# Kernel optimization log

Hardware: AMD Instinct MI355X
Metric: run time of the kernel (lower is better)

The kernel has to match this reference:

```python
import jax, jax.numpy as jnp
import numpy as np

N_H = 896
N_EMB = 300
V_IN = 30000
V_OUT = 30000
B = 64
T_ENC = 40
T_DEC = 40


def gru_cell(x, h, Wih, Whh, bih, bhh):
    # PyTorch GRU cell math
    gi = x @ Wih.T + bih          # [B, 3H]
    gh = h @ Whh.T + bhh          # [B, 3H]
    ir, iz, inn = jnp.split(gi, 3, axis=-1)
    hr, hz, hn = jnp.split(gh, 3, axis=-1)
    r = jax.nn.sigmoid(ir + hr)
    z = jax.nn.sigmoid(iz + hz)
    n = jnp.tanh(inn + r * hn)
    return (1.0 - z) * n + z * h


def run_gru(xs, h0, Wih, Whh, bih, bhh, reverse=False):
    # xs: [T, B, E] -> outputs [T, B, H], final hidden [B, H]
    def step(h, x):
        h2 = gru_cell(x, h, Wih, Whh, bih, bhh)
        return h2, h2
    hT, ys = jax.lax.scan(step, h0, xs, reverse=reverse)
    return ys, hT


def setup_inputs() -> dict:
    key = jax.random.key(0)
    ks = jax.random.split(key, 20)
    s = 0.05
    inp = {
        'x_encoder': jax.random.randint(ks[0], (B, T_ENC), 0, V_IN - 1),
        'x_decoder': jax.random.randint(ks[1], (B, T_DEC), 0, V_OUT - 1),
        'emb_enc': jax.random.normal(ks[2], (V_IN, N_EMB), jnp.float32) * s,
        'Wih_f': jax.random.normal(ks[3], (3 * N_H, N_EMB), jnp.float32) * s,
        'Whh_f': jax.random.normal(ks[4], (3 * N_H, N_H), jnp.float32) * s,
        'bih_f': jnp.zeros((3 * N_H,), jnp.float32),
        'bhh_f': jnp.zeros((3 * N_H,), jnp.float32),
        'Wih_b': jax.random.normal(ks[5], (3 * N_H, N_EMB), jnp.float32) * s,
        'Whh_b': jax.random.normal(ks[6], (3 * N_H, N_H), jnp.float32) * s,
        'bih_b': jnp.zeros((3 * N_H,), jnp.float32),
        'bhh_b': jnp.zeros((3 * N_H,), jnp.float32),
        'emb_dec': jax.random.normal(ks[7], (V_OUT, N_EMB), jnp.float32) * s,
        'Wih_d': jax.random.normal(ks[8], (3 * N_H, N_EMB), jnp.float32) * s,
        'Whh_d': jax.random.normal(ks[9], (3 * N_H, N_H), jnp.float32) * s,
        'bih_d': jnp.zeros((3 * N_H,), jnp.float32),
        'bhh_d': jnp.zeros((3 * N_H,), jnp.float32),
        'fc_W': jax.random.normal(ks[10], (V_OUT, 2 * N_H), jnp.float32) * s,
        'fc_b': jnp.zeros((V_OUT,), jnp.float32),
    }
    return inp


def reference(x_encoder, x_decoder, emb_enc, Wih_f, Whh_f, bih_f, bhh_f,
              Wih_b, Whh_b, bih_b, bhh_b, emb_dec, Wih_d, Whh_d, bih_d,
              bhh_d, fc_W, fc_b):
    Bsz = x_encoder.shape[0]
    h0 = jnp.zeros((Bsz, N_H), jnp.float32)

    # ---- Encoder: bidirectional 1-layer GRU (no padding, full lengths) ----
    xs = emb_enc[x_encoder].transpose(1, 0, 2)          # [Te, B, E]
    y_f, h_f = run_gru(xs, h0, Wih_f, Whh_f, bih_f, bhh_f)
    y_b, h_b = run_gru(xs, h0, Wih_b, Whh_b, bih_b, bhh_b, reverse=True)
    y_enc = (y_f + y_b).transpose(1, 0, 2)              # [B, Te, H] (dirs summed)
    h = h_f + h_b                                       # [B, H]

    # ---- Decoder: per-step GRU + dot-product attention over encoder ----
    xd = emb_dec[x_decoder].transpose(1, 0, 2)          # [Td, B, E]

    def dec_step(h, x):
        h2 = gru_cell(x, h, Wih_d, Whh_d, bih_d, bhh_d)        # [B, H]
        scores = jnp.einsum('bth,bh->bt', y_enc, h2)           # ed_mat
        attn = jax.nn.softmax(scores, axis=1)                  # over Te
        ctx = jnp.einsum('bt,bth->bh', attn, y_enc)            # [B, H]
        logits = jnp.concatenate([h2, ctx], axis=-1) @ fc_W.T + fc_b
        return h2, jax.nn.softmax(logits, axis=-1)

    _, ys = jax.lax.scan(dec_step, h, xd)               # [Td, B, V]
    return ys.transpose(1, 0, 2)                        # [B, Td, V]
```

## Files before the change

### kernel.cpp

```cpp
#include <hip/hip_runtime.h>

#define BB 64
#define TE 40
#define TD 40
#define ED 300
#define EP 320
#define HD 896
#define G3 2688
#define VO 30000
#define VP2 30208
#define KZ 1792
#define KT 28
#define MR 2560
#define NBLK 120
#define NWB 248
#define NTN 118
#define NTILE (NTN * 10)

#define FOFF 0
#define BOFF 56
#define DOFF 112
#define AOFF 168
#define TOFF 232
#define ZOFF 352
#define QOFF 448
#define FWC  456
#define MTO  464
#define QSO  496
#define FSTR 32

typedef __attribute__((ext_vector_type(8))) __bf16 bf16x8;
typedef __attribute__((ext_vector_type(4))) float f32x4;
typedef __attribute__((ext_vector_type(4))) unsigned int u32x4;
typedef __attribute__((ext_vector_type(4))) unsigned short u16x4;

typedef __attribute__((address_space(1))) const void av1c;
typedef __attribute__((address_space(3))) void av3;

__device__ __forceinline__ float sig_(float x)  { return 1.0f / (1.0f + __expf(-x)); }
__device__ __forceinline__ float tanh_(float x) { return 1.0f - 2.0f / (__expf(2.0f * x) + 1.0f); }

__device__ __forceinline__ void gload_lds16(const __bf16* g, __bf16* l) {
    __builtin_amdgcn_global_load_lds((av1c*)g, (av3*)l, 16, 0, 0);
}
__device__ __forceinline__ void gload_lds16_sc(const __bf16* g, __bf16* l) {
    __builtin_amdgcn_global_load_lds((av1c*)g, (av3*)l, 16, 0, 17);
}

__device__ __forceinline__ bf16x8 ld128_sc(const __bf16* p) {
    bf16x8 r;
    asm volatile("global_load_dwordx4 %0, %1, off sc0 sc1" : "=v"(r) : "v"(p));
    return r;
}
__device__ __forceinline__ f32x4 ldf4_sc(const float* p) {
    f32x4 r;
    asm volatile("global_load_dwordx4 %0, %1, off sc0 sc1" : "=v"(r) : "v"(p));
    return r;
}
__device__ __forceinline__ float ldf_sc(const float* p) {
    float r;
    asm volatile("global_load_dword %0, %1, off sc0 sc1" : "=v"(r) : "v"(p));
    return r;
}
__device__ __forceinline__ void vm_wait0() {
    asm volatile("s_waitcnt vmcnt(0)" ::: "memory");
}
__device__ __forceinline__ void stf_sc(float* p, float v) {
    asm volatile("global_store_dword %0, %1, off sc0 sc1" :: "v"(p), "v"(v) : "memory");
}
__device__ __forceinline__ void sth_sc(__bf16* p, float v) {
    unsigned int u = (unsigned int)__builtin_bit_cast(unsigned short, (__bf16)v);
    asm volatile("global_store_short %0, %1, off sc0 sc1" :: "v"(p), "v"(u) : "memory");
}
__device__ __forceinline__ void st8_sc(__bf16* p, u16x4 v) {
    asm volatile("global_store_dwordx2 %0, %1, off sc0 sc1" :: "v"(p), "v"(v) : "memory");
}
__device__ __forceinline__ void sti_sc(int* p, int v) {
    asm volatile("global_store_dword %0, %1, off sc0 sc1" :: "v"(p), "v"(v) : "memory");
}
__device__ __forceinline__ void spin_ge(const int* p, int target) {
    int v;
    for (;;) {
        asm volatile("global_load_dword %0, %1, off sc0 sc1\n\ts_waitcnt vmcnt(0)"
                     : "=v"(v) : "v"(p) : "memory");
        if (v >= target) break;
        __builtin_amdgcn_s_sleep(1);
    }
}
__device__ __forceinline__ void spinb(const int* p, int target) {
    for (int it = 0; it < (1 << 20); ++it) {
        int v;
        asm volatile("global_load_dword %0, %1, off sc0 sc1\n\ts_waitcnt vmcnt(0)"
                     : "=v"(v) : "v"(p) : "memory");
        if (v >= target) return;
        __builtin_amdgcn_s_sleep(16);
    }
}

__device__ __forceinline__ size_t hblk(int b, int c) {
    return ((size_t)(c >> 4) * 64 + b) * 16 + (c & 15);
}

__device__ __forceinline__ void stage_w(__bf16* wlds, const float* __restrict__ W, int c0)
{
    const int tid = threadIdx.x;
    for (int ch = tid; ch < 48 * 224; ch += 256) {
        const int lr = ch / 224, c4 = (ch % 224) * 4;
        const int g = lr >> 4, rr = lr & 15;
        const int kk = c4 >> 5, hi = (c4 & 31) >> 3, j = c4 & 7;
        const float4 v = *(const float4*)&W[(size_t)(g * HD + c0 + rr) * HD + c4];
        __bf16* d = &wlds[((g * 28 + kk) * 64 + hi * 16 + rr) * 8 + j];
        d[0] = (__bf16)v.x; d[1] = (__bf16)v.y; d[2] = (__bf16)v.z; d[3] = (__bf16)v.w;
    }
}

struct GiReg { float g0[4], g1[4], g2[4]; };

__device__ __forceinline__ GiReg gi_prefetch(const float* __restrict__ GIt,
                                             int c, int w, int hi)
{
    GiReg r;
#pragma unroll
    for (int rg = 0; rg < 4; ++rg) {
        const float* gp = GIt + (size_t)(16 * w + hi * 4 + rg) * G3 + c;
        r.g0[rg] = gp[0]; r.g1[rg] = gp[HD]; r.g2[rg] = gp[2 * HD];
    }
    return r;
}

__device__ __forceinline__ void gru_step(
    const __bf16* __restrict__ hcurB, const float* __restrict__ hcurF,
    const __bf16* __restrict__ wlds, const GiReg& gi,
    float bh0, float bh1, float bh2,
    float* __restrict__ hnF, __bf16* __restrict__ hnB,
    float* __restrict__ yencD, int tt,
    __bf16* __restrict__ zrow,
    int c0, int lane, int w)
{
    const int r16 = lane & 15, hi = lane >> 4;
    const int c = c0 + r16;
    const int colblk = c0 >> 4;
    const int brow = 16 * w;

    bf16x8 afr[28];
    const __bf16* ap = hcurB + ((size_t)(hi >> 1) * 64 + brow + r16) * 16 + (hi & 1) * 8;
#pragma unroll
    for (int kk = 0; kk < 28; ++kk) afr[kk] = ld128_sc(ap + kk * 2048);
    float hp[4];
#pragma unroll
    for (int rg = 0; rg < 4; ++rg)
        hp[rg] = ldf_sc(hcurF + ((size_t)colblk * 64 + brow + hi * 4 + rg) * 16 + r16);
    vm_wait0();
    __builtin_amdgcn_sched_barrier(0);

    f32x4 a0 = {0.f, 0.f, 0.f, 0.f}, a1 = a0, a2 = a0;
#pragma unroll
    for (int kk = 0; kk < 28; ++kk) {
        const bf16x8 b0 = *(const bf16x8*)&wlds[(kk) * 512 + lane * 8];
        const bf16x8 b1 = *(const bf16x8*)&wlds[(28 + kk) * 512 + lane * 8];
        const bf16x8 b2 = *(const bf16x8*)&wlds[(56 + kk) * 512 + lane * 8];
        a0 = __builtin_amdgcn_mfma_f32_16x16x32_bf16(afr[kk], b0, a0, 0, 0, 0);
        a1 = __builtin_amdgcn_mfma_f32_16x16x32_bf16(afr[kk], b1, a1, 0, 0, 0);
        a2 = __builtin_amdgcn_mfma_f32_16x16x32_bf16(afr[kk], b2, a2, 0, 0, 0);
    }

#pragma unroll
    for (int rg = 0; rg < 4; ++rg) {
        const int b = brow + hi * 4 + rg;
        const float rr = sig_(gi.g0[rg] + a0[rg] + bh0);
        const float zz = sig_(gi.g1[rg] + a1[rg] + bh1);
        const float nn = tanh_(gi.g2[rg] + rr * (a2[rg] + bh2));
        const float hnew = (1.0f - zz) * nn + zz * hp[rg];
        const size_t so = ((size_t)colblk * 64 + b) * 16 + r16;
        stf_sc(hnF + so, hnew);
        sth_sc(hnB + so, hnew);
        if (yencD) stf_sc(yencD + (((size_t)colblk * 64 + b) * TE + tt) * 16 + r16, hnew);
        if (zrow)  sth_sc(zrow + (size_t)b * KZ + c, hnew);
    }
}

__device__ __forceinline__ void attn_step512(
    const float* __restrict__ yencL, float* __restrict__ h2s,
    float* __restrict__ scL, float* __restrict__ attwL,
    const float* __restrict__ h2g, int b, __bf16* __restrict__ zr,
    int* __restrict__ myflag, int* __restrict__ zflag, int postval)
{
    const int tid = threadIdx.x, lane = tid & 63, w = tid >> 6;

    float a0 = 0.f, a1 = 0.f;
    if (tid < HD) a0 = ldf_sc(h2g + hblk(b, tid));
    if (tid + 512 < HD) a1 = ldf_sc(h2g + hblk(b, tid + 512));
    vm_wait0();
    __builtin_amdgcn_sched_barrier(0);
    if (tid < HD) h2s[tid] = a0;
    if (tid + 512 < HD) h2s[tid + 512] = a1;
    __syncthreads();
    if (tid == 0) sti_sc(myflag, postval);

    const float2* h22 = (const float2*)h2s;
    for (int t = w; t < TE; t += 8) {
        const float2* y2 = (const float2*)(yencL + t * HD);
        float p = 0.f;
#pragma unroll
        for (int it = 0; it < HD / 128; ++it) {
            const float2 ya = y2[lane + it * 64];
            const float2 hb2 = h22[lane + it * 64];
            p += ya.x * hb2.x + ya.y * hb2.y;
        }
        p += __shfl_down(p, 32); p += __shfl_down(p, 16); p += __shfl_down(p, 8);
        p += __shfl_down(p, 4);  p += __shfl_down(p, 2);  p += __shfl_down(p, 1);
        if (lane == 0) scL[t] = p;
    }
    __syncthreads();

    float m = scL[0];
    for (int t = 1; t < TE; ++t) m = fmaxf(m, scL[t]);
    float s = 0.f;
    for (int t = 0; t < TE; ++t) s += __expf(scL[t] - m);
    const float inv = 1.0f / s;
    if (tid < TE) attwL[tid] = __expf(scL[tid] - m) * inv;
    __syncthreads();

    for (int c = tid; c < HD; c += 512) {
        float acc = 0.f;
#pragma unroll
        for (int t = 0; t < TE; ++t) acc += attwL[t] * yencL[t * HD + c];
        sth_sc(zr + (size_t)b * KZ + HD + c, acc);
    }
    vm_wait0();
    __syncthreads();
    if (tid == 0) sti_sc(zflag, postval);
}

__device__ __forceinline__ void softmax512(float* row, float* red, float* red2,
                                           float* __restrict__ orow)
{
    const int tid = threadIdx.x, lane = tid & 63, w = tid >> 6;

    for (int it = 0; it < 3; ++it) {
        f32x4 v[5]; int jj[5]; bool ok[5];
#pragma unroll
        for (int u = 0; u < 5; ++u) {
            jj[u] = it * 2560 + u * 512 + tid;
            ok[u] = jj[u] < VO / 4;
            if (ok[u]) v[u] = ldf4_sc(orow + (size_t)jj[u] * 4);
        }
        vm_wait0();
        __builtin_amdgcn_sched_barrier(0);
#pragma unroll
        for (int u = 0; u < 5; ++u)
            if (ok[u]) *(f32x4*)&row[(size_t)jj[u] * 4] = v[u];
    }
    __syncthreads();

    float m = -1e30f;
    for (int ch = tid; ch < VO / 4; ch += 512) {
        const f32x4 x = *(const f32x4*)&row[ch * 4];
        m = fmaxf(fmaxf(fmaxf(m, x[0]), x[1]), fmaxf(x[2], x[3]));
    }
    m = fmaxf(m, __shfl_down(m, 32)); m = fmaxf(m, __shfl_down(m, 16));
    m = fmaxf(m, __shfl_down(m, 8));  m = fmaxf(m, __shfl_down(m, 4));
    m = fmaxf(m, __shfl_down(m, 2));  m = fmaxf(m, __shfl_down(m, 1));
    if (lane == 0) red[w] = m;
    __syncthreads();
    if (tid == 0) {
        float mm = red[0];
#pragma unroll
        for (int i = 1; i < 8; ++i) mm = fmaxf(mm, red[i]);
        red[0] = mm;
    }
    __syncthreads();
    m = red[0];

    float s = 0.0f;
    for (int v2 = tid; v2 < VO; v2 += 512) {
        const float e = __expf(row[v2] - m);
        row[v2] = e;
        s += e;
    }
    s += __shfl_down(s, 32); s += __shfl_down(s, 16); s += __shfl_down(s, 8);
    s += __shfl_down(s, 4);  s += __shfl_down(s, 2);  s += __shfl_down(s, 1);
    if (lane == 0) red2[w] = s;
    __syncthreads();
    if (tid == 0) {
        float ss = red2[0];
#pragma unroll
        for (int i = 1; i < 8; ++i) ss += red2[i];
        red2[0] = ss;
    }
    __syncthreads();
    s = red2[0];

    const float inv = 1.0f / s;
    for (int ch = tid; ch < VO / 4; ch += 512) {
        f32x4 x = *(const f32x4*)&row[ch * 4];
        x[0] *= inv; x[1] *= inv; x[2] *= inv; x[3] *= inv;
        *(f32x4*)&orow[(size_t)ch * 4] = x;
    }
    __syncthreads();
}

__global__ __launch_bounds__(512, 1) void recur(
    const float* __restrict__ GIf, const float* __restrict__ GIb,
    const float* __restrict__ GId,
    const float* __restrict__ WhhF, const float* __restrict__ WhhB,
    const float* __restrict__ WhhD,
    const float* __restrict__ bhhF, const float* __restrict__ bhhB,
    const float* __restrict__ bhhD,
    float* __restrict__ heF, __bf16* __restrict__ heB,
    float* __restrict__ hdF, __bf16* __restrict__ hdB,
    float* __restrict__ yenc_f, float* __restrict__ yenc_b,
    __bf16* __restrict__ Zb, int* __restrict__ flags,
    const float* __restrict__ fcWsrc, __bf16* __restrict__ fcW,
    float* __restrict__ outC, const float* __restrict__ fcb)
{
    __shared__ __align__(16) char smem[147456];
    __bf16* wlds  = (__bf16*)smem;
    float*  yencL = (float*)smem;
    float*  h2s   = (float*)(smem + 143360);
    float*  scL   = (float*)(smem + 146944);
    float*  attwL = (float*)(smem + 147136);
    float*  redA  = (float*)(smem + 131072);
    float*  redB  = (float*)(smem + 131136);
    volatile int* shtile = (volatile int*)(smem + 147400);

    const int gid = blockIdx.x;
    const int tid = threadIdx.x;
    const int lane = tid & 63, w = tid >> 6;
    const int r16 = lane & 15, hi = lane >> 4;
    const size_t S = (size_t)BB * HD;

    if (gid < NBLK) {
        float bb0 = 0.f, bb1 = 0.f, bb2 = 0.f;
        GiReg gi;

        if (gid < 112) {
            const int dir = (gid >= 56) ? 1 : 0;
            const int gloc = dir ? gid - 56 : gid;
            const int c0e = gloc * 16;
            const float* GIe  = dir ? GIb : GIf;
            const float* bhhE = dir ? bhhB : bhhF;
            float* yencD = dir ? yenc_b : yenc_f;
            const int foff = dir ? BOFF : FOFF;
            const int ce = c0e + r16;

            stage_w(wlds, dir ? WhhB : WhhF, c0e);
            if (tid < 256) {
                bb0 = bhhE[ce]; bb1 = bhhE[HD + ce]; bb2 = bhhE[2 * HD + ce];
                gi = gi_prefetch(GIe + (size_t)(dir ? TE - 1 : 0) * BB * G3, ce, w, hi);
            }
            __syncthreads();

            for (int t = 0; t < TE; ++t) {
                if (t > 0) {
                    if (tid < 56) spin_ge(flags + (foff + tid) * FSTR, t);
                    __syncthreads();
                }
                const int tt = dir ? (TE - 1 - t) : t;
                if (tid < 256)
                    gru_step(heB + (size_t)(dir * 2 + (t & 1)) * S,
                             heF + (size_t)(dir * 2 + (t & 1)) * S,
                             wlds, gi, bb0, bb1, bb2,
                             heF + (size_t)(dir * 2 + ((t + 1) & 1)) * S,
                             heB + (size_t)(dir * 2 + ((t + 1) & 1)) * S,
                             yencD, tt, nullptr, c0e, lane, w);
                vm_wait0();
                __syncthreads();
                if (tid == 0) sti_sc(flags + (foff + gloc) * FSTR, t + 1);
                if (t + 1 < TE && tid < 256) {
                    const int ttn = dir ? (TE - 2 - t) : (t + 1);
                    gi = gi_prefetch(GIe + (size_t)ttn * BB * G3, ce, w, hi);
                }
            }
        }

        if (tid < 112) spin_ge(flags + tid * FSTR, TE);
        __syncthreads();

        {
            const int i0 = gid * 256 + tid;
            const int i1 = i0 + NBLK * 256;
            const bool has0 = (i0 < BB * HD);
            const bool has1 = (i1 < BB * HD);
            const float f0 = has0 ? ldf_sc(&heF[0 * S + i0]) : 0.f;
            const float b0 = has0 ? ldf_sc(&heF[2 * S + i0]) : 0.f;
            const float f1 = has1 ? ldf_sc(&heF[0 * S + i1]) : 0.f;
            const float b1 = has1 ? ldf_sc(&heF[2 * S + i1]) : 0.f;
            vm_wait0();
            __builtin_amdgcn_sched_barrier(0);
            if (has0) { const float v0 = f0 + b0; stf_sc(&hdF[i0], v0); sth_sc(&hdB[i0], v0); }
            if (has1) { const float v1 = f1 + b1; stf_sc(&hdF[i1], v1); sth_sc(&hdB[i1], v1); }
        }
        if (gid < 56) {
            stage_w(wlds, WhhD, gid * 16);
            if (tid < 256) {
                const int cd = gid * 16 + r16;
                bb0 = bhhD[cd]; bb1 = bhhD[HD + cd]; bb2 = bhhD[2 * HD + cd];
                gi = gi_prefetch(GId, cd, w, hi);
            }
        }
        vm_wait0();
        __syncthreads();
        if (tid == 0) sti_sc(flags + (TOFF + gid) * FSTR, 1);
        if (tid < 120) spin_ge(flags + (TOFF + tid) * FSTR, 1);
        __syncthreads();

        if (gid < 56) {
            for (int p = 0; p < TD; ++p) {
                if (p > 0 && tid < 56) spin_ge(flags + (DOFF + tid) * FSTR, p);
                if (p >= 4 && tid >= 64 && tid < 128)
                    spin_ge(flags + (AOFF + tid - 64) * FSTR, p - 3);
                __syncthreads();
                if (tid < 256)
                    gru_step(hdB + (size_t)(p & 3) * S, hdF + (size_t)(p & 3) * S,
                             wlds, gi, bb0, bb1, bb2,
                             hdF + (size_t)((p + 1) & 3) * S, hdB + (size_t)((p + 1) & 3) * S,
                             nullptr, 0, Zb + (size_t)p * BB * KZ, gid * 16, lane, w);
                vm_wait0();
                __syncthreads();
                if (tid == 0) sti_sc(flags + (DOFF + gid) * FSTR, p + 1);
                if (p + 1 < TD && tid < 256)
                    gi = gi_prefetch(GId + (size_t)(p + 1) * BB * G3, gid * 16 + r16, w, hi);
            }
        } else {
            const int b = gid - 56;
            const float* sf = yenc_f;
            const float* sb = yenc_b;
            for (int it = 0; it < 4; ++it) {
                f32x4 a_[5], b_[5];
                int tt_[5], gg_[5], cc_[5]; bool ok[5];
#pragma unroll
                for (int u = 0; u < 5; ++u) {
                    const int j = it * 2560 + u * 512 + tid;
                    ok[u] = (j < 8960);
                    if (ok[u]) {
                        gg_[u] = j / 160;
                        const int rem = j - gg_[u] * 160;
                        tt_[u] = rem >> 2;
                        cc_[u] = (rem & 3) * 4;
                        const size_t sa = (((size_t)gg_[u] * 64 + b) * TE + tt_[u]) * 16 + cc_[u];
                        a_[u] = ldf4_sc(sf + sa);
                        b_[u] = ldf4_sc(sb + sa);
                    }
                }
                vm_wait0();
                __builtin_amdgcn_sched_barrier(0);
#pragma unroll
                for (int u = 0; u < 5; ++u)
                    if (ok[u])
                        *(f32x4*)&yencL[(size_t)tt_[u] * HD + gg_[u] * 16 + cc_[u]] = a_[u] + b_[u];
            }
            __syncthreads();
            for (int s = 0; s < TD; ++s) {
                if (tid < 56) spin_ge(flags + (DOFF + tid) * FSTR, s + 1);
                __syncthreads();
                attn_step512(yencL, h2s, scL, attwL, hdF + (size_t)((s + 1) & 3) * S,
                             b, Zb + (size_t)s * BB * KZ,
                             flags + (AOFF + b) * FSTR, flags + (ZOFF + b) * FSTR, s + 1);
            }
        }
    } else {
        const int slice = gid - NBLK;
        const size_t base = (size_t)slice * 236 * KZ;
        const int nf4 = 236 * KZ / 4;
        for (int i = tid; i < nf4; i += 512) {
            const size_t e0 = base + (size_t)i * 4;
            const int r = (int)(e0 / KZ);
            u16x4 o;
            if (r < VO) {
                const float4 x = *(const float4*)&fcWsrc[e0];
                o.x = __builtin_bit_cast(unsigned short, (__bf16)x.x);
                o.y = __builtin_bit_cast(unsigned short, (__bf16)x.y);
                o.z = __builtin_bit_cast(unsigned short, (__bf16)x.z);
                o.w = __builtin_bit_cast(unsigned short, (__bf16)x.w);
            } else {
                o.x = 0; o.y = 0; o.z = 0; o.w = 0;
            }
            st8_sc(&fcW[e0], o);
        }
        vm_wait0();
        __syncthreads();
        if (tid == 0)
            __hip_atomic_fetch_add(flags + FWC * FSTR, 1, __ATOMIC_RELAXED,
                                   __HIP_MEMORY_SCOPE_AGENT);
    }

    {
        __bf16* lds = (__bf16*)smem;
        const int wave = tid >> 6;
        const int wm = wave >> 2, wn = wave & 3;
        int* qcnt = flags + QOFF * FSTR;

        if (tid == 0) spinb(flags + FWC * FSTR, 128);
        __syncthreads();

        const int srow0 = wave * 8 + (lane >> 3);
        const int scol  = ((lane & 7) ^ (lane >> 3)) * 8;
        const int cbx0 = ((hi * 16) ^ ((r16 & 7) << 4)) >> 1;
        const int cbx1 = ((64 + hi * 16) ^ ((r16 & 7) << 4)) >> 1;

        for (;;) {
            if (tid == 0) {
                const int tl = __hip_atomic_fetch_add(qcnt, 1, __ATOMIC_RELAXED,
                                                      __HIP_MEMORY_SCOPE_AGENT);
                *shtile = tl;
            }
            __syncthreads();
            const int tile = *shtile;
            if (tile >= NTILE) break;
            const int mt = tile / NTN, nt = tile - mt * NTN;
            const int need = 4 * mt + 4;
            if (tid < 56) spinb(flags + (DOFF + tid) * FSTR, need);
            if (tid >= 64 && tid < 128) spinb(flags + (ZOFF + tid - 64) * FSTR, need);
            __syncthreads();

            const long tileM = (long)mt * 256;
            const long tileN = (long)nt * 256;
            const __bf16* gAh[2] = { Zb + (size_t)tileM * KZ, Zb + (size_t)(tileM + 128) * KZ };
            const __bf16* gBh[2] = { fcW + (size_t)tileN * KZ, fcW + (size_t)(tileN + 128) * KZ };
            auto Abase = [](int buf, int h) { return (buf * 2 + h) * 8192; };
            auto Bbase = [](int buf, int h) { return 32768 + (buf * 2 + h) * 8192; };
            auto stageA = [&](const __bf16* gph, int kt, int lbase) {
                const __bf16* g0 = gph + (size_t)srow0 * KZ + kt * 64 + scol;
                gload_lds16_sc(g0, &lds[lbase + wave * 512]);
                gload_lds16_sc(g0 + (size_t)64 * KZ, &lds[lbase + (8 + wave) * 512]);
            };
            auto stageB = [&](const __bf16* gph, int kt, int lbase) {
                const __bf16* g0 = gph + (size_t)srow0 * KZ + kt * 64 + scol;
                gload_lds16(g0, &lds[lbase + wave * 512]);
                gload_lds16(g0 + (size_t)64 * KZ, &lds[lbase + (8 + wave) * 512]);
            };

            f32x4 acc[8][4];
            const f32x4 zero = {0.f, 0.f, 0.f, 0.f};
#pragma unroll
            for (int m = 0; m < 8; ++m)
#pragma unroll
                for (int n = 0; n < 4; ++n) acc[m][n] = zero;

            stageA(gAh[0], 0, Abase(0, 0));
            stageA(gAh[1], 0, Abase(0, 1));
            stageB(gBh[0], 0, Bbase(0, 0));
            stageB(gBh[1], 0, Bbase(0, 1));
            stageB(gBh[0], 1, Bbase(1, 0));
            stageB(gBh[1], 1, Bbase(1, 1));
            asm volatile("s_waitcnt vmcnt(4)" ::: "memory");
            __builtin_amdgcn_s_barrier();

            for (int kt = 0; kt < KT; ++kt) {
                const int buf = kt & 1;
                const int kn1 = (kt + 1 < KT) ? kt + 1 : 0;
                const int kn2 = (kt + 2 < KT) ? kt + 2 : 0;
                const int Ab = Abase(buf, wm);
                const int Bb = Bbase(buf, wn >> 1);
                bf16x8 bfr[4][2];
#pragma unroll
                for (int q = 0; q < 4; ++q) {
                    if (q == 0) {
#pragma unroll
                        for (int n = 0; n < 4; ++n) {
                            const int rowB = (wn & 1) * 64 + n * 16 + r16;
                            bfr[n][0] = *(const bf16x8*)&lds[Bb + rowB * 64 + cbx0];
                            bfr[n][1] = *(const bf16x8*)&lds[Bb + rowB * 64 + cbx1];
                        }
                    }
                    bf16x8 af[2][2];
#pragma unroll
                    for (int mm = 0; mm < 2; ++mm) {
                        const int rowA = (q * 2 + mm) * 16 + r16;
                        af[mm][0] = *(const bf16x8*)&lds[Ab + rowA * 64 + cbx0];
                        af[mm][1] = *(const bf16x8*)&lds[Ab + rowA * 64 + cbx1];
                    }
                    if (q == 0)      stageA(gAh[0], kn1, Abase(buf ^ 1, 0));
                    else if (q == 1) stageA(gAh[1], kn1, Abase(buf ^ 1, 1));
                    else if (q == 2) stageB(gBh[0], kn2, Bbase(buf, 0));
                    else {
                        stageB(gBh[1], kn2, Bbase(buf, 1));
                        asm volatile("s_waitcnt vmcnt(4)" ::: "memory");
                    }
                    __builtin_amdgcn_s_barrier();
                    asm volatile("s_waitcnt lgkmcnt(0)" ::: "memory");
                    __builtin_amdgcn_sched_barrier(0);
                    __builtin_amdgcn_s_setprio(1);
#pragma unroll
                    for (int mm = 0; mm < 2; ++mm)
#pragma unroll
                        for (int n = 0; n < 4; ++n) {
                            acc[q * 2 + mm][n] = __builtin_amdgcn_mfma_f32_16x16x32_bf16(
                                af[mm][0], bfr[n][0], acc[q * 2 + mm][n], 0, 0, 0);
                            acc[q * 2 + mm][n] = __builtin_amdgcn_mfma_f32_16x16x32_bf16(
                                af[mm][1], bfr[n][1], acc[q * 2 + mm][n], 0, 0, 0);
                        }
                    __builtin_amdgcn_s_setprio(0);
                    __builtin_amdgcn_sched_barrier(0);
                    __builtin_amdgcn_s_barrier();
                }
            }
            asm volatile("s_waitcnt vmcnt(0)" ::: "memory");

#pragma unroll
            for (int m = 0; m < 8; ++m) {
#pragma unroll
                for (int n = 0; n < 4; ++n) {
                    const long gcol = tileN + wn * 64 + n * 16 + r16;
                    if (gcol >= VO) continue;
                    const float bv = fcb[gcol];
#pragma unroll
                    for (int rr = 0; rr < 4; ++rr) {
                        const long grow = tileM + wm * 128 + m * 16 + hi * 4 + rr;
                        const long t = grow >> 6, b = grow & 63;
                        stf_sc(&outC[(b * TD + t) * VO + gcol], acc[m][n][rr] + bv);
                    }
                }
            }
            vm_wait0();
            __syncthreads();
            if (tid == 0)
                __hip_atomic_fetch_add(flags + (MTO + mt) * FSTR, 1, __ATOMIC_RELAXED,
                                       __HIP_MEMORY_SCOPE_AGENT);
            __syncthreads();
        }
    }

    {
        int* qs = flags + QSO * FSTR;
        for (;;) {
            if (tid == 0) {
                const int qv = __hip_atomic_fetch_add(qs, 1, __ATOMIC_RELAXED,
                                                      __HIP_MEMORY_SCOPE_AGENT);
                *shtile = qv;
            }
            __syncthreads();
            const int q = *shtile;
            if (q >= MR) break;
            const int mt = q >> 8;
            if (tid == 0) spinb(flags + (MTO + mt) * FSTR, NTN);
            __syncthreads();
            const int sub = q & 255;
            const int t = 4 * mt + (sub >> 6), b = sub & 63;
            softmax512((float*)smem, redA, redB, outC + (size_t)(b * TD + t) * VO);
        }
    }
}

__global__ __launch_bounds__(256) void gemm_bt(
    const __bf16* __restrict__ A0, const __bf16* __restrict__ B0,
    float* __restrict__ C0, const float* __restrict__ bias0,
    const __bf16* __restrict__ A1, const __bf16* __restrict__ B1,
    float* __restrict__ C1, const float* __restrict__ bias1,
    int M, int N, int K)
{
    constexpr int BM = 128, BN = 128, BK = 32;
    constexpr int FM = 4, FN = 4;

    const __bf16* A = A0; const __bf16* Bp = B0;
    float* C = C0; const float* bias = bias0;
    if (blockIdx.z == 1) { A = A1; Bp = B1; C = C1; bias = bias1; }

    __shared__ __bf16 Ash[2][BM * BK];
    __shared__ __bf16 Bsh[2][BN * BK];

    const int tid  = threadIdx.x;
    const int lane = tid & 63;
    const int wave = tid >> 6;
    const int wr = wave >> 1, wc = wave & 1;

    const int nwg = gridDim.x * gridDim.y;
    const int orig = blockIdx.y * gridDim.x + blockIdx.x;
    const int q = nwg >> 3, r = nwg & 7;
    const int xcd = orig & 7, idx = orig >> 3;
    const int wg = (xcd < r ? xcd * (q + 1) : r * (q + 1) + (xcd - r) * q) + idx;
    const int mtiles = gridDim.y;
    const long tileM = (long)(wg % mtiles) * BM;
    const long tileN = (long)(wg / mtiles) * BN;

    const int r16 = lane & 15;
    const int hi  = lane >> 4;

    f32x4 acc[FM][FN];
    const f32x4 zero = {0.f, 0.f, 0.f, 0.f};
#pragma unroll
    for (int m = 0; m < FM; ++m)
#pragma unroll
        for (int n = 0; n < FN; ++n) acc[m][n] = zero;

    const int srow = wave * 32 + (lane >> 2);
    const int schunk = (lane & 3) * 8;
    const __bf16* gA = A + (size_t)(tileM + srow) * K + schunk;
    const __bf16* gB = Bp + (size_t)(tileN + srow) * K + schunk;
    const size_t kstep16 = (size_t)16 * K;
    const int lofs = (wave * 32) * BK;

#define STAGE_T(k0_, sel_)                                            \
    do {                                                              \
        gload_lds16(gA + (k0_), &Ash[sel_][lofs]);                    \
        gload_lds16(gA + (k0_) + kstep16, &Ash[sel_][lofs + 16 * BK]);\
        gload_lds16(gB + (k0_), &Bsh[sel_][lofs]);                    \
        gload_lds16(gB + (k0_) + kstep16, &Bsh[sel_][lofs + 16 * BK]);\
    } while (0)

    STAGE_T(0, 0);
    int cur = 0;
    for (int k0 = BK; k0 < K; k0 += BK) {
        STAGE_T(k0, cur ^ 1);
        asm volatile("s_waitcnt vmcnt(4)" ::: "memory");
        __builtin_amdgcn_s_barrier();
        __builtin_amdgcn_sched_barrier(0);

        bf16x8 af[FM], bfr[FN];
#pragma unroll
        for (int m = 0; m < FM; ++m)
            af[m] = *(const bf16x8*)&Ash[cur][(wr * 64 + m * 16 + r16) * BK + hi * 8];
#pragma unroll
        for (int n = 0; n < FN; ++n)
            bfr[n] = *(const bf16x8*)&Bsh[cur][(wc * 64 + n * 16 + r16) * BK + hi * 8];
#pragma unroll
        for (int m = 0; m < FM; ++m)
#pragma unroll
            for (int n = 0; n < FN; ++n)
                acc[m][n] = __builtin_amdgcn_mfma_f32_16x16x32_bf16(af[m], bfr[n], acc[m][n], 0, 0, 0);

        __builtin_amdgcn_sched_barrier(0);
        __builtin_amdgcn_s_barrier();
        __builtin_amdgcn_sched_barrier(0);
        cur ^= 1;
    }
    asm volatile("s_waitcnt vmcnt(0)" ::: "memory");
    __builtin_amdgcn_s_barrier();
    __builtin_amdgcn_sched_barrier(0);
    {
        bf16x8 af[FM], bfr[FN];
#pragma unroll
        for (int m = 0; m < FM; ++m)
            af[m] = *(const bf16x8*)&Ash[cur][(wr * 64 + m * 16 + r16) * BK + hi * 8];
#pragma unroll
        for (int n = 0; n < FN; ++n)
            bfr[n] = *(const bf16x8*)&Bsh[cur][(wc * 64 + n * 16 + r16) * BK + hi * 8];
#pragma unroll
        for (int m = 0; m < FM; ++m)
#pragma unroll
            for (int n = 0; n < FN; ++n)
                acc[m][n] = __builtin_amdgcn_mfma_f32_16x16x32_bf16(af[m], bfr[n], acc[m][n], 0, 0, 0);
    }
#undef STAGE_T

#pragma unroll
    for (int m = 0; m < FM; ++m) {
#pragma unroll
        for (int n = 0; n < FN; ++n) {
            const long gcol = tileN + wc * 64 + n * 16 + r16;
            const float bv = bias ? bias[gcol] : 0.0f;
#pragma unroll
            for (int rr = 0; rr < 4; ++rr) {
                const long grow = tileM + wr * 64 + m * 16 + hi * 4 + rr;
                C[grow * N + gcol] = acc[m][n][rr] + bv;
            }
        }
    }
}

__global__ __launch_bounds__(256) void conv_pad(const float* __restrict__ src,
                                                __bf16* __restrict__ dst,
                                                int Rout, int Rin, int Kout, int Kin)
{
    size_t i = (size_t)blockIdx.x * 256 + threadIdx.x;
    const size_t total = (size_t)Rout * Kout;
    const size_t stride = (size_t)gridDim.x * 256;
    for (; i < total; i += stride) {
        int k = (int)(i % Kout);
        int r = (int)(i / Kout);
        float v = (r < Rin && k < Kin) ? src[(size_t)r * Kin + k] : 0.0f;
        dst[i] = (__bf16)v;
    }
}

__global__ __launch_bounds__(256) void gather_embed(const int* __restrict__ tok,
                                                    const float* __restrict__ emb,
                                                    __bf16* __restrict__ X)
{
    int i = blockIdx.x * 256 + threadIdx.x;
    const int total = TE * BB * EP;
    for (; i < total; i += gridDim.x * 256) {
        int e = i % EP;
        int row = i / EP;
        int t = row >> 6, b = row & 63;
        float v = 0.0f;
        if (e < ED) v = emb[(size_t)tok[b * TE + t] * ED + e];
        X[i] = (__bf16)v;
    }
}

extern "C" void kernel_launch(void* const* d_in, const int* in_sizes, int n_in,
                              void* d_out, int out_size, void* d_ws, size_t ws_size,
                              hipStream_t stream)
{
    if (n_in < 18) return;
    const int*   x_enc   = (const int*)d_in[0];
    const int*   x_dec   = (const int*)d_in[1];
    const float* emb_enc = (const float*)d_in[2];
    const float* Wih_f   = (const float*)d_in[3];
    const float* Whh_f   = (const float*)d_in[4];
    const float* bih_f   = (const float*)d_in[5];
    const float* bhh_f   = (const float*)d_in[6];
    const float* Wih_b   = (const float*)d_in[7];
    const float* Whh_b   = (const float*)d_in[8];
    const float* bih_b   = (const float*)d_in[9];
    const float* bhh_b   = (const float*)d_in[10];
    const float* emb_dec = (const float*)d_in[11];
    const float* Wih_d   = (const float*)d_in[12];
    const float* Whh_d   = (const float*)d_in[13];
    const float* bih_d   = (const float*)d_in[14];
    const float* bhh_d   = (const float*)d_in[15];
    const float* fc_W    = (const float*)d_in[16];
    const float* fc_b    = (const float*)d_in[17];
    float* out = (float*)d_out;

    size_t off = 0;
    auto alloc = [&](size_t bytes) -> void* {
        void* p = (char*)d_ws + off;
        off = (off + bytes + 255) & ~(size_t)255;
        return p;
    };
    __bf16* fcWb   = (__bf16*)alloc((size_t)VP2 * KZ * 2);
    __bf16* WihFb  = (__bf16*)alloc((size_t)G3 * EP * 2);
    __bf16* WihBb  = (__bf16*)alloc((size_t)G3 * EP * 2);
    __bf16* WihDb  = (__bf16*)alloc((size_t)G3 * EP * 2);
    __bf16* Xe     = (__bf16*)alloc((size_t)MR * EP * 2);
    __bf16* Xd     = (__bf16*)alloc((size_t)MR * EP * 2);
    float*  GIf    = (float*)alloc((size_t)MR * G3 * 4);
    float*  GIb    = (float*)alloc((size_t)MR * G3 * 4);
    float*  GId    = (float*)alloc((size_t)MR * G3 * 4);
    __bf16* Zb     = (__bf16*)alloc((size_t)MR * KZ * 2);
    float*  yenc_f = (float*)alloc((size_t)BB * TE * HD * 4);
    float*  yenc_b = (float*)alloc((size_t)BB * TE * HD * 4);
    float*  hdF    = (float*)alloc((size_t)4 * BB * HD * 4);
    __bf16* hdB    = (__bf16*)alloc((size_t)4 * BB * HD * 2);
    char* zero_start = (char*)d_ws + off;
    float*  heF    = (float*)alloc((size_t)4 * BB * HD * 4);
    __bf16* heB    = (__bf16*)alloc((size_t)4 * BB * HD * 2);
    int*    flags  = (int*)alloc(512 * FSTR * 4);
    size_t zero_bytes = (size_t)(((char*)d_ws + off) - zero_start);
    if (off > ws_size) return;

    hipMemsetAsync(zero_start, 0, zero_bytes, stream);
    conv_pad<<<3360, 256, 0, stream>>>(Wih_f, WihFb, G3, G3, EP, ED);
    conv_pad<<<3360, 256, 0, stream>>>(Wih_b, WihBb, G3, G3, EP, ED);
    conv_pad<<<3360, 256, 0, stream>>>(Wih_d, WihDb, G3, G3, EP, ED);
    gather_embed<<<3200, 256, 0, stream>>>(x_enc, emb_enc, Xe);
    gather_embed<<<3200, 256, 0, stream>>>(x_dec, emb_dec, Xd);

    gemm_bt<<<dim3(G3 / 128, MR / 128, 2), 256, 0, stream>>>(
        Xe, WihFb, GIf, bih_f, Xe, WihBb, GIb, bih_b, MR, G3, EP);
    gemm_bt<<<dim3(G3 / 128, MR / 128, 1), 256, 0, stream>>>(
        Xd, WihDb, GId, bih_d, nullptr, nullptr, nullptr, nullptr, MR, G3, EP);

    recur<<<NWB, 512, 0, stream>>>(GIf, GIb, GId, Whh_f, Whh_b, Whh_d,
                                   bhh_f, bhh_b, bhh_d,
                                   heF, heB, hdF, hdB, yenc_f, yenc_b, Zb, flags,
                                   fc_W, fcWb, out, fc_b);
}
```

Before: 915.4 us.

## Interleave softmax rows into the FC tile work queue per M-tile

Merges the separate softmax work queue into the FC GEMM tile queue. Each M-tile group now holds its 118 GEMM tiles followed by 256 softmax row items, so softmax for earlier time steps overlaps with GEMM tiles of later steps instead of waiting for all GEMMs to finish. The cost is that blocks grabbing a softmax item may spin until every tile of that M-tile has completed, which can stall blocks that could otherwise do GEMM work.

Measured after the change: 1.303 ms. 42.3% more time.

```diff
diff --git a/kernel.cpp b/kernel.cpp
--- a/kernel.cpp
+++ b/kernel.cpp
@@ -15,7 +15,8 @@
 #define NBLK 120
 #define NWB 248
 #define NTN 118
-#define NTILE (NTN * 10)
+#define GITEM (NTN + 256)
+#define NITEM (10 * GITEM)
 
 #define FOFF 0
 #define BOFF 56
@@ -26,7 +27,6 @@
 #define QOFF 448
 #define FWC  456
 #define MTO  464
-#define QSO  496
 #define FSTR 32
 
 typedef __attribute__((ext_vector_type(8))) __bf16 bf16x8;
@@ -506,9 +506,21 @@
                 *shtile = tl;
             }
             __syncthreads();
-            const int tile = *shtile;
-            if (tile >= NTILE) break;
-            const int mt = tile / NTN, nt = tile - mt * NTN;
+            const int item = *shtile;
+            if (item >= NITEM) break;
+            const int mt = item / GITEM;
+            const int sub = item - mt * GITEM;
+
+            if (sub >= NTN) {
+                const int r = sub - NTN;
+                if (tid == 0) spinb(flags + (MTO + mt) * FSTR, NTN);
+                __syncthreads();
+                const int t = 4 * mt + (r >> 6), b = r & 63;
+                softmax512((float*)smem, redA, redB, outC + (size_t)(b * TD + t) * VO);
+                continue;
+            }
+
+            const int nt = sub;
             const int need = 4 * mt + 4;
             if (tid < 56) spinb(flags + (DOFF + tid) * FSTR, need);
             if (tid >= 64 && tid < 128) spinb(flags + (ZOFF + tid - 64) * FSTR, need);
@@ -619,26 +631,6 @@
                 __hip_atomic_fetch_add(flags + (MTO + mt) * FSTR, 1, __ATOMIC_RELAXED,
                                        __HIP_MEMORY_SCOPE_AGENT);
             __syncthreads();
-        }
-    }
-
-    {
-        int* qs = flags + QSO * FSTR;
-        for (;;) {
-            if (tid == 0) {
-                const int qv = __hip_atomic_fetch_add(qs, 1, __ATOMIC_RELAXED,
-                                                      __HIP_MEMORY_SCOPE_AGENT);
-                *shtile = qv;
-            }
-            __syncthreads();
-            const int q = *shtile;
-            if (q >= MR) break;
-            const int mt = q >> 8;
-            if (tid == 0) spinb(flags + (MTO + mt) * FSTR, NTN);
-            __syncthreads();
-            const int sub = q & 255;
-            const int t = 4 * mt + (sub >> 6), b = sub & 63;
-            softmax512((float*)smem, redA, redB, outC + (size_t)(b * TD + t) * VO);
         }
     }
 }
```
